# Kernel optimization log

Hardware: AMD Instinct MI355X
Metric: run time of the kernel (lower is better)

Reference implementation:

```python
import jax, jax.numpy as jnp
import numpy as np
from jax import lax

# ConvTranspose2d(stride=1, padding=p) == conv with spatially-flipped, in/out-swapped
# weight and padding k-1-p per side. Here k=3, p=1 -> conv padding (1,1).
K = 3
P = 1
_CONV_PAD = K - 1 - P  # = 1

def _rconv(a, w):
    # a: [N,C,H,Wf] real, w: [O,I,kH,kW]
    return lax.conv_general_dilated(
        a, w, window_strides=(1, 1),
        padding=[(_CONV_PAD, _CONV_PAD), (_CONV_PAD, _CONV_PAD)],
        dimension_numbers=("NCHW", "OIHW", "NCHW"))


def setup_inputs() -> dict:
    key = jax.random.key(0)
    k1, k2, k3, k4, k5 = jax.random.split(key, 5)
    N, C_IN, C_OUT, H, W = 8, 16, 16, 512, 512
    x = jax.random.normal(k1, (N, C_IN, H, W), dtype=jnp.float32)
    # torch ConvTranspose2d weight layout: (in, out, kH, kW), complex64 split into re/im
    scale = 1.0 / np.sqrt(C_IN * K * K)
    w_real = jax.random.normal(k2, (C_IN, C_OUT, K, K), dtype=jnp.float32) * scale
    w_imag = jax.random.normal(k3, (C_IN, C_OUT, K, K), dtype=jnp.float32) * scale
    b_real = jax.random.normal(k4, (C_OUT,), dtype=jnp.float32) * scale
    b_imag = jax.random.normal(k5, (C_OUT,), dtype=jnp.float32) * scale
    return {"x": x, "w_real": w_real, "w_imag": w_imag, "b_real": b_real, "b_imag": b_imag}


def reference(x, w_real, w_imag, b_real, b_imag):
    # rfftn over last two dims (norm='backward')
    X = jnp.fft.rfftn(x, axes=(-2, -1), norm="backward")  # [N,C,H,W//2+1] complex64
    Xr, Xi = jnp.real(X), jnp.imag(X)
    # convert transpose-conv weight to equivalent conv weight: flip spatial, swap in/out
    wr = jnp.transpose(jnp.flip(w_real, axis=(-2, -1)), (1, 0, 2, 3))
    wi = jnp.transpose(jnp.flip(w_imag, axis=(-2, -1)), (1, 0, 2, 3))
    # complex conv via real/imag decomposition
    Yr = _rconv(Xr, wr) - _rconv(Xi, wi) + b_real[:, None, None]
    Yi = _rconv(Xr, wi) + _rconv(Xi, wr) + b_imag[:, None, None]
    Y = lax.complex(Yr, Yi)
    # irfftn with no explicit s: last dim -> 2*(Wf-1) = W
    return jnp.fft.irfftn(Y, axes=(-2, -1), norm="backward")
```

## Files before the change

### kernel.cpp

```cpp
#include <hip/hip_runtime.h>
#include <math.h>

#define PI_F 3.14159265358979323846f

#define FI(i) ((i) + ((i) >> 4))
#define CSTRIDE 544
#define TSTRIDE 546

__device__ inline float2 cmulf(float2 a, float2 b) {
    return make_float2(a.x * b.x - a.y * b.y, a.x * b.y + a.y * b.x);
}
__device__ inline float2 cadd(float2 a, float2 b) { return make_float2(a.x + b.x, a.y + b.y); }
__device__ inline float2 csub(float2 a, float2 b) { return make_float2(a.x - b.x, a.y - b.y); }

__device__ inline void cmac(float2& a, float2 w, float2 v) {
    a.x = fmaf(w.x, v.x, a.x);
    a.x = fmaf(-w.y, v.y, a.x);
    a.y = fmaf(w.x, v.y, a.y);
    a.y = fmaf(w.y, v.x, a.y);
}

__device__ inline int xcd_remap(int bid, int q) {
    return (bid & 7) * q + (bid >> 3);
}

__device__ inline void build_tbl128(float2* tbl, int tid) {
    if (tid < 128) {
        float ang = -2.0f * PI_F * (float)tid * (1.0f / 512.0f);
        tbl[tid] = make_float2(cosf(ang), sinf(ang));
    }
}

template <int NCOLS>
__device__ inline float2* fft512_r4(float2* a, float2* b, const float2* tbl, int tid, bool inv) {
    const int bf = tid & 127;
    const int cp = tid >> 7;
#pragma unroll
    for (int st = 0; st < 4; ++st) {
        const int slog = 2 * st;
        const int s = 1 << slog;
        const int p = bf >> slog;
        const int q = bf & (s - 1);
        float2 w1 = tbl[p << slog];
        if (inv) w1.y = -w1.y;
        const float2 w2 = cmulf(w1, w1);
        const float2 w3 = cmulf(w2, w1);
        const int i0 = bf;
        const int ob = q + (p << (slog + 2));
#pragma unroll
        for (int t = 0; t < NCOLS / 2; ++t) {
            const int cc = cp + 2 * t;
            const float2* ac = a + cc * CSTRIDE;
            float2* bc = b + cc * CSTRIDE;
            float2 A = ac[FI(i0)];
            float2 B = ac[FI(i0 + 128)];
            float2 C = ac[FI(i0 + 256)];
            float2 D = ac[FI(i0 + 384)];
            float2 apc = cadd(A, C), amc = csub(A, C);
            float2 bpd = cadd(B, D), bmd = csub(B, D);
            float2 jb = make_float2(-bmd.y, bmd.x);
            if (inv) { jb.x = -jb.x; jb.y = -jb.y; }
            bc[FI(ob)]           = cadd(apc, bpd);
            bc[FI(ob + s)]       = cmulf(csub(amc, jb), w1);
            bc[FI(ob + 2 * s)]   = cmulf(csub(apc, bpd), w2);
            bc[FI(ob + 3 * s)]   = cmulf(cadd(amc, jb), w3);
        }
        __syncthreads();
        float2* tmp = a; a = b; b = tmp;
    }
    {
#pragma unroll
        for (int cc = 0; cc < NCOLS; ++cc) {
            const float2* ac = a + cc * CSTRIDE;
            float2* bc = b + cc * CSTRIDE;
            float2 A = ac[FI(tid)];
            float2 B = ac[FI(tid + 256)];
            bc[FI(tid)]       = cadd(A, B);
            bc[FI(tid + 256)] = csub(A, B);
        }
        __syncthreads();
        float2* tmp = a; a = b; b = tmp;
    }
    return a;
}

__device__ inline void wave_fence() {
    asm volatile("s_waitcnt lgkmcnt(0)" ::: "memory");
    __builtin_amdgcn_sched_barrier(0);
}

template <bool INV>
__device__ inline float2 rot90(float2 z) {
    return INV ? make_float2(-z.y, z.x) : make_float2(z.y, -z.x);
}

template <bool INV>
__device__ inline void dft8(float2 v[8]) {
    const float R2 = 0.70710678118654752f;
    float2 t0 = cadd(v[0], v[4]), t1 = csub(v[0], v[4]);
    float2 t2 = cadd(v[2], v[6]), t3 = csub(v[2], v[6]);
    float2 s0 = cadd(v[1], v[5]), s1 = csub(v[1], v[5]);
    float2 s2 = cadd(v[3], v[7]), s3 = csub(v[3], v[7]);
    float2 rt3 = rot90<INV>(t3), rs3 = rot90<INV>(s3);
    float2 E0 = cadd(t0, t2), E1 = cadd(t1, rt3), E2 = csub(t0, t2), E3 = csub(t1, rt3);
    float2 O0 = cadd(s0, s2), O1 = cadd(s1, rs3), O2 = csub(s0, s2), O3 = csub(s1, rs3);
    float2 rO1 = rot90<INV>(O1), rO2 = rot90<INV>(O2), rO3 = rot90<INV>(O3);
    float2 a1 = make_float2(R2 * (O1.x + rO1.x), R2 * (O1.y + rO1.y));
    float2 a2 = rO2;
    float2 a3 = make_float2(R2 * (rO3.x - O3.x), R2 * (rO3.y - O3.y));
    v[0] = cadd(E0, O0); v[4] = csub(E0, O0);
    v[1] = cadd(E1, a1); v[5] = csub(E1, a1);
    v[2] = cadd(E2, a2); v[6] = csub(E2, a2);
    v[3] = cadd(E3, a3); v[7] = csub(E3, a3);
}

__device__ inline void twiddle8(float2 v[8], float2 w1) {
    float2 w2 = cmulf(w1, w1);
    float2 w3 = cmulf(w2, w1);
    float2 w4 = cmulf(w2, w2);
    float2 w5 = cmulf(w4, w1);
    float2 w6 = cmulf(w3, w3);
    float2 w7 = cmulf(w4, w3);
    v[1] = cmulf(v[1], w1); v[2] = cmulf(v[2], w2); v[3] = cmulf(v[3], w3);
    v[4] = cmulf(v[4], w4); v[5] = cmulf(v[5], w5); v[6] = cmulf(v[6], w6);
    v[7] = cmulf(v[7], w7);
}

template <bool INV>
__device__ inline void fft512_wave_ip(float2 v[8], float2* R, int lane) {
    const float sg = INV ? (6.2831853071795865f / 512.0f)
                         : (-6.2831853071795865f / 512.0f);
    float2 w1;
    __sincosf(sg * (float)lane, &w1.y, &w1.x);
    dft8<INV>(v);
    twiddle8(v, w1);
#pragma unroll
    for (int m = 0; m < 8; ++m) R[FI(8 * lane + m)] = v[m];
    wave_fence();
#pragma unroll
    for (int j = 0; j < 8; ++j) v[j] = R[FI(lane + 64 * j)];
    float2 w1b;
    w1b.x = __shfl(w1.x, lane & 56);
    w1b.y = __shfl(w1.y, lane & 56);
    dft8<INV>(v);
    twiddle8(v, w1b);
    {
        int ob = (lane & 7) + ((lane >> 3) << 6);
#pragma unroll
        for (int m = 0; m < 8; ++m) R[FI(ob + 8 * m)] = v[m];
    }
    wave_fence();
#pragma unroll
    for (int j = 0; j < 8; ++j) v[j] = R[FI(lane + 64 * j)];
    dft8<INV>(v);
}

__global__ __launch_bounds__(256) void k_row_rfft(const float* __restrict__ x,
                                                  float2* __restrict__ G) {
    __shared__ float2 b0[4 * CSTRIDE], b1[4 * CSTRIDE], tbl[128];
    int tid = threadIdx.x;
    int nc = blockIdx.x >> 7;
    int h0 = (blockIdx.x & 127) * 4;
    build_tbl128(tbl, tid);
    const float4* xr = (const float4*)(x + ((size_t)nc * 512 + h0) * 512);
#pragma unroll
    for (int j = 0; j < 2; ++j) {
        int t4 = tid + 256 * j;
        float4 v = xr[t4];
        int e = t4 * 4;
        int k = e >> 9, i = e & 511;
        float2* dst = b0 + k * CSTRIDE + FI(i);
        dst[0] = make_float2(v.x, 0.0f);
        dst[1] = make_float2(v.y, 0.0f);
        dst[2] = make_float2(v.z, 0.0f);
        dst[3] = make_float2(v.w, 0.0f);
    }
    __syncthreads();
    float2* res = fft512_r4<4>(b0, b1, tbl, tid, false);
#pragma unroll
    for (int k = 0; k < 4; ++k) {
        float2* g = G + ((size_t)(nc * 512 + h0 + k)) * 257;
        g[tid] = res[k * CSTRIDE + FI(tid)];
        if (tid == 0) g[256] = res[k * CSTRIDE + FI(256)];
    }
}

__global__ __launch_bounds__(1024) void k_col_fft(const float2* __restrict__ G,
                                                  float2* __restrict__ XT) {
    __shared__ float2 tile[16][TSTRIDE];
    int tid = threadIdx.x;
    int l = xcd_remap(blockIdx.x, 272);
    int nc = l / 17;
    int v0 = (l % 17) * 16;
#pragma unroll
    for (int j = 0; j < 8; ++j) {
        int e = tid + 1024 * j;
        int dv = e & 15, h = e >> 4;
        int v = v0 + dv;
        float2 val = make_float2(0.0f, 0.0f);
        if (v < 257) val = G[((size_t)nc * 512 + h) * 257 + v];
        tile[dv][FI(h)] = val;
    }
    __syncthreads();
    int lane = tid & 63, w = tid >> 6;
    float2* R = tile[w];
    float2 vv[8];
#pragma unroll
    for (int j = 0; j < 8; ++j) vv[j] = R[FI(lane + 64 * j)];
    fft512_wave_ip<false>(vv, R, lane);
    int v = v0 + w;
    if (v < 257) {
        float2* dst = XT + ((size_t)nc * 257 + v) * 512;
#pragma unroll
        for (int m = 0; m < 8; ++m) dst[lane + 64 * m] = vv[m];
    }
}

__global__ __launch_bounds__(256, 4) void k_conv(const float2* __restrict__ XT,
                                                 float2* __restrict__ YT,
                                                 const float* __restrict__ wr,
                                                 const float* __restrict__ wi,
                                                 const float* __restrict__ br,
                                                 const float* __restrict__ bi) {
    __shared__ float2 Xs[16 * 4 * 66];
    int tid = threadIdx.x;
    int bid = blockIdx.x;
    int ut = bid & 7;
    int rest = bid >> 3;
    int vt = rest % 129;
    int n = rest / 129;
    int u0 = ut * 64;
    int v0 = vt * 2;

    for (int l = tid; l < 4224; l += 256) {
        int c = l / 264;
        int rem = l - c * 264;
        int dvr = rem / 66;
        int uu = rem - dvr * 66;
        int vg = v0 - 1 + dvr;
        int ug = u0 - 1 + uu;
        float2 val = make_float2(0.0f, 0.0f);
        if (vg >= 0 && vg < 257 && ug >= 0 && ug < 512)
            val = XT[(((size_t)n * 16 + c) * 257 + vg) * 512 + ug];
        Xs[l] = val;
    }
    __syncthreads();

    int lane = tid & 63;
    int wv = __builtin_amdgcn_readfirstlane(tid >> 6);
    int o0 = wv * 4;

    float2 acc[2][4];
#pragma unroll
    for (int oo = 0; oo < 4; ++oo) {
        float2 bv = make_float2(br[o0 + oo], bi[o0 + oo]);
        acc[0][oo] = bv;
        acc[1][oo] = bv;
    }

    for (int c = 0; c < 16; ++c) {
        float2 xv[4][3];
#pragma unroll
        for (int dvr = 0; dvr < 4; ++dvr) {
            const float2* row = &Xs[(c * 4 + dvr) * 66];
            xv[dvr][0] = row[lane];
            xv[dvr][1] = row[lane + 1];
            xv[dvr][2] = row[lane + 2];
        }
#pragma unroll
        for (int oo = 0; oo < 4; ++oo) {
            const float* wrp = wr + ((size_t)(c * 16 + o0 + oo)) * 9;
            const float* wip = wi + ((size_t)(c * 16 + o0 + oo)) * 9;
            float wre[9], wim[9];
#pragma unroll
            for (int t = 0; t < 9; ++t) { wre[t] = wrp[t]; wim[t] = wip[t]; }
#pragma unroll
            for (int kw = 0; kw < 3; ++kw) {
#pragma unroll
                for (int kh = 0; kh < 3; ++kh) {
                    int t = kh * 3 + kw;
                    int xj = 2 - kh;
                    float2 w = make_float2(wre[t], wim[t]);
                    cmac(acc[0][oo], w, xv[2 - kw][xj]);
                    cmac(acc[1][oo], w, xv[3 - kw][xj]);
                }
            }
        }
    }

#pragma unroll
    for (int oo = 0; oo < 4; ++oo) {
#pragma unroll
        for (int vv = 0; vv < 2; ++vv) {
            int v = v0 + vv;
            if (v < 257)
                YT[(((size_t)n * 16 + o0 + oo) * 257 + v) * 512 + u0 + lane] =
                    acc[vv][oo];
        }
    }
}

__global__ __launch_bounds__(256) void k_col_ifft(const float2* __restrict__ YT,
                                                  float2* __restrict__ ZT) {
    __shared__ float2 b0[4 * CSTRIDE], b1[4 * CSTRIDE], tbl[128];
    int tid = threadIdx.x;
    int no = blockIdx.x / 65;
    int v0 = (blockIdx.x % 65) * 4;
    build_tbl128(tbl, tid);
#pragma unroll
    for (int k = 0; k < 4; ++k) {
        int v = v0 + k;
        const float2* src = YT + ((size_t)no * 257 + (v < 257 ? v : 256)) * 512;
        b0[k * CSTRIDE + FI(tid)]       = src[tid];
        b0[k * CSTRIDE + FI(tid + 256)] = src[tid + 256];
    }
    __syncthreads();
    float2* res = fft512_r4<4>(b0, b1, tbl, tid, true);
    const float sc = 1.0f / 512.0f;
#pragma unroll
    for (int k = 0; k < 4; ++k) {
        int v = v0 + k;
        if (v < 257) {
            float2* dst = ZT + ((size_t)no * 257 + v) * 512;
            float2 r0 = res[k * CSTRIDE + FI(tid)];
            float2 r1 = res[k * CSTRIDE + FI(tid + 256)];
            dst[tid]       = make_float2(r0.x * sc, r0.y * sc);
            dst[tid + 256] = make_float2(r1.x * sc, r1.y * sc);
        }
    }
}

__global__ __launch_bounds__(1024) void k_row_irfft(const float2* __restrict__ ZT,
                                                    float* __restrict__ out) {
    __shared__ float2 tile[16][TSTRIDE];
    int tid = threadIdx.x;
    int no = blockIdx.x >> 5;
    int h0 = (blockIdx.x & 31) * 16;
#pragma unroll
    for (int j = 0; j < 5; ++j) {
        int e = tid + 1024 * j;
        if (e < 4112) {
            int dh = e & 15, vv = e >> 4;
            tile[dh][FI(vv)] = ZT[((size_t)no * 257 + vv) * 512 + h0 + dh];
        }
    }
    __syncthreads();
    int lane = tid & 63, w = tid >> 6;
    float2* R = tile[w];
    float2 v[8];
#pragma unroll
    for (int j = 0; j < 8; ++j) {
        int i = lane + 64 * j;
        float2 val;
        if (i <= 256) {
            val = R[FI(i)];
            if (i == 0 || i == 256) val.y = 0.0f;
        } else {
            val = R[FI(512 - i)];
            val.y = -val.y;
        }
        v[j] = val;
    }
    fft512_wave_ip<true>(v, R, lane);
    const float sc = 1.0f / 512.0f;
    float* dst = out + ((size_t)no * 512 + h0 + w) * 512;
#pragma unroll
    for (int m = 0; m < 8; ++m) dst[lane + 64 * m] = v[m].x * sc;
}

extern "C" void kernel_launch(void* const* d_in, const int* in_sizes, int n_in,
                              void* d_out, int out_size, void* d_ws, size_t ws_size,
                              hipStream_t stream) {
    const float* x  = (const float*)d_in[0];
    const float* wr = (const float*)d_in[1];
    const float* wi = (const float*)d_in[2];
    const float* br = (const float*)d_in[3];
    const float* bi = (const float*)d_in[4];
    float* out = (float*)d_out;

    const size_t bufElems = (size_t)128 * 257 * 512;
    float2* A = (float2*)d_ws;
    float2* B = A + bufElems;

    k_row_rfft<<<128 * 128, 256, 0, stream>>>(x, A);
    k_col_fft<<<128 * 17, 1024, 0, stream>>>(A, B);
    k_conv<<<8 * 129 * 8, 256, 0, stream>>>(B, A, wr, wi, br, bi);
    k_col_ifft<<<128 * 65, 256, 0, stream>>>(A, B);
    k_row_irfft<<<128 * 32, 1024, 0, stream>>>(B, out);
}
```

Before: 637.6 us.

## Pack two real rows into one complex FFT for row rfft and irfft

```diff
diff --git a/kernel.cpp b/kernel.cpp
--- a/kernel.cpp
+++ b/kernel.cpp
@@ -157,31 +157,44 @@
 
 __global__ __launch_bounds__(256) void k_row_rfft(const float* __restrict__ x,
                                                   float2* __restrict__ G) {
-    __shared__ float2 b0[4 * CSTRIDE], b1[4 * CSTRIDE], tbl[128];
-    int tid = threadIdx.x;
-    int nc = blockIdx.x >> 7;
-    int h0 = (blockIdx.x & 127) * 4;
-    build_tbl128(tbl, tid);
-    const float4* xr = (const float4*)(x + ((size_t)nc * 512 + h0) * 512);
-#pragma unroll
-    for (int j = 0; j < 2; ++j) {
-        int t4 = tid + 256 * j;
-        float4 v = xr[t4];
-        int e = t4 * 4;
-        int k = e >> 9, i = e & 511;
-        float2* dst = b0 + k * CSTRIDE + FI(i);
-        dst[0] = make_float2(v.x, 0.0f);
-        dst[1] = make_float2(v.y, 0.0f);
-        dst[2] = make_float2(v.z, 0.0f);
-        dst[3] = make_float2(v.w, 0.0f);
-    }
-    __syncthreads();
-    float2* res = fft512_r4<4>(b0, b1, tbl, tid, false);
-#pragma unroll
-    for (int k = 0; k < 4; ++k) {
-        float2* g = G + ((size_t)(nc * 512 + h0 + k)) * 257;
-        g[tid] = res[k * CSTRIDE + FI(tid)];
-        if (tid == 0) g[256] = res[k * CSTRIDE + FI(256)];
+    __shared__ float2 lds[4][544];
+    int lane = threadIdx.x & 63;
+    int w = threadIdx.x >> 6;
+    int pair = blockIdx.x * 4 + w;
+    const float* x0 = x + (size_t)(2 * pair) * 512;
+    const float* x1 = x0 + 512;
+    float2 v[8];
+#pragma unroll
+    for (int j = 0; j < 8; ++j)
+        v[j] = make_float2(x0[lane + 64 * j], x1[lane + 64 * j]);
+    fft512_wave_ip<false>(v, lds[w], lane);
+    float2 P[5];
+#pragma unroll
+    for (int m = 0; m < 5; ++m) {
+        int src = (64 - lane) & 63;
+        float2 p;
+        p.x = __shfl(v[7 - m].x, src);
+        p.y = __shfl(v[7 - m].y, src);
+        if (lane == 0) p = v[(8 - m) & 7];
+        P[m] = p;
+    }
+    float2* g0 = G + (size_t)(2 * pair) * 257;
+    float2* g1 = g0 + 257;
+#pragma unroll
+    for (int m = 0; m < 4; ++m) {
+        int k = lane + 64 * m;
+        float2 Z = v[m], Pc = P[m];
+        float2 S = make_float2(0.5f * (Z.x + Pc.x), 0.5f * (Z.y - Pc.y));
+        float2 D = make_float2(Z.x - Pc.x, Z.y + Pc.y);
+        float2 T = make_float2(0.5f * D.y, -0.5f * D.x);
+        g0[k] = S;
+        g1[k] = T;
+    }
+    if (lane == 0) {
+        float2 Z = v[4], Pc = P[4];
+        g0[256] = make_float2(0.5f * (Z.x + Pc.x), 0.5f * (Z.y - Pc.y));
+        float2 D = make_float2(Z.x - Pc.x, Z.y + Pc.y);
+        g1[256] = make_float2(0.5f * D.y, -0.5f * D.x);
     }
 }
 
@@ -330,15 +343,15 @@
     }
 }
 
-__global__ __launch_bounds__(1024) void k_row_irfft(const float2* __restrict__ ZT,
-                                                    float* __restrict__ out) {
+__global__ __launch_bounds__(512) void k_row_irfft(const float2* __restrict__ ZT,
+                                                   float* __restrict__ out) {
     __shared__ float2 tile[16][TSTRIDE];
     int tid = threadIdx.x;
     int no = blockIdx.x >> 5;
     int h0 = (blockIdx.x & 31) * 16;
 #pragma unroll
-    for (int j = 0; j < 5; ++j) {
-        int e = tid + 1024 * j;
+    for (int j = 0; j < 9; ++j) {
+        int e = tid + 512 * j;
         if (e < 4112) {
             int dh = e & 15, vv = e >> 4;
             tile[dh][FI(vv)] = ZT[((size_t)no * 257 + vv) * 512 + h0 + dh];
@@ -346,26 +359,35 @@
     }
     __syncthreads();
     int lane = tid & 63, w = tid >> 6;
-    float2* R = tile[w];
+    float2* Ra = tile[2 * w];
+    float2* Rb = tile[2 * w + 1];
     float2 v[8];
 #pragma unroll
-    for (int j = 0; j < 8; ++j) {
-        int i = lane + 64 * j;
-        float2 val;
+    for (int m = 0; m < 8; ++m) {
+        int i = lane + 64 * m;
+        float2 a, b, W;
         if (i <= 256) {
-            val = R[FI(i)];
-            if (i == 0 || i == 256) val.y = 0.0f;
+            a = Ra[FI(i)];
+            b = Rb[FI(i)];
+            if (i == 0 || i == 256) { a.y = 0.0f; b.y = 0.0f; }
+            W = make_float2(a.x - b.y, a.y + b.x);
         } else {
-            val = R[FI(512 - i)];
-            val.y = -val.y;
-        }
-        v[j] = val;
-    }
-    fft512_wave_ip<true>(v, R, lane);
+            int ii = 512 - i;
+            a = Ra[FI(ii)];
+            b = Rb[FI(ii)];
+            W = make_float2(a.x + b.y, -a.y + b.x);
+        }
+        v[m] = W;
+    }
+    fft512_wave_ip<true>(v, Ra, lane);
     const float sc = 1.0f / 512.0f;
-    float* dst = out + ((size_t)no * 512 + h0 + w) * 512;
-#pragma unroll
-    for (int m = 0; m < 8; ++m) dst[lane + 64 * m] = v[m].x * sc;
+    float* d0 = out + ((size_t)no * 512 + h0 + 2 * w) * 512;
+    float* d1 = d0 + 512;
+#pragma unroll
+    for (int m = 0; m < 8; ++m) {
+        d0[lane + 64 * m] = v[m].x * sc;
+        d1[lane + 64 * m] = v[m].y * sc;
+    }
 }
 
 extern "C" void kernel_launch(void* const* d_in, const int* in_sizes, int n_in,
@@ -382,9 +404,9 @@
     float2* A = (float2*)d_ws;
     float2* B = A + bufElems;
 
-    k_row_rfft<<<128 * 128, 256, 0, stream>>>(x, A);
+    k_row_rfft<<<8192, 256, 0, stream>>>(x, A);
     k_col_fft<<<128 * 17, 1024, 0, stream>>>(A, B);
     k_conv<<<8 * 129 * 8, 256, 0, stream>>>(B, A, wr, wi, br, bi);
     k_col_ifft<<<128 * 65, 256, 0, stream>>>(A, B);
-    k_row_irfft<<<128 * 32, 1024, 0, stream>>>(B, out);
-}
+    k_row_irfft<<<128 * 32, 512, 0, stream>>>(B, out);
+}
```

New measurement: 615.9 us. 3.4% less time.
